# Optimization experiments

Measured on AMD Instinct MI355X. Metric: run time of the kernel, lower is better.

## Reference

```python
import jax, jax.numpy as jnp
import numpy as np

T, E, K, H, I = 1024, 8, 2, 1024, 2048  # tokens, experts, top_k, hidden, intermediate


def setup_inputs() -> dict:
    key = jax.random.key(0)
    k1, k2, k3, k4, k5 = jax.random.split(key, 5)
    x = jax.random.normal(k1, (T, H), dtype=jnp.float32)
    router_logits = jax.random.normal(k2, (T, E), dtype=jnp.float32)
    # expert weights: w1/w3 = gate/up proj (E,H,I); w2 = down proj (E,I,H)
    w1 = jax.random.normal(k3, (E, H, I), dtype=jnp.float32) / np.float32(np.sqrt(H))
    w3 = jax.random.normal(k4, (E, H, I), dtype=jnp.float32) / np.float32(np.sqrt(H))
    w2 = jax.random.normal(k5, (E, I, H), dtype=jnp.float32) / np.float32(np.sqrt(I))
    return {"x": x, "router_logits": router_logits, "w1": w1, "w3": w3, "w2": w2}


def reference(x, router_logits, w1, w3, w2):
    # --- fused top-k router (renormalize_topk_logits=False) ---
    probs = jax.nn.softmax(router_logits, axis=-1)          # [T, E]
    top_vals, top_ids = jax.lax.top_k(probs, K)             # [T, K]
    t_idx = jnp.arange(probs.shape[0])[:, None]
    # sparse combine weights scattered back to dense [T, E] (per-row ids are unique)
    gate = jnp.zeros_like(probs).at[t_idx, top_ids].add(top_vals)
    # --- expert FFN: silu(x@w1) * (x@w3) @ w2, masked by gate ---
    h = jnp.einsum('th,ehi->tei', x, w1)                    # [T, E, I]
    u = jnp.einsum('th,ehi->tei', x, w3)                    # [T, E, I]
    a = jax.nn.silu(h) * u                                  # [T, E, I]
    y = jnp.einsum('tei,eio->teo', a, w2)                   # [T, E, H]
    out = jnp.einsum('te,teo->to', gate, y)                 # [T, H]
    return out
```

## Files before the change

### kernel.cpp

```cpp
#include <hip/hip_runtime.h>

#define T_TOK 1024
#define NEXP 8
#define HID 1024
#define INTER 2048
#define SLOT_CAP 2176
#define NSLOT 2048
#define MAXTILES 24

#define BK 32
#define SPLITK 2
#define KCHUNK (INTER / SPLITK)

typedef __bf16 bf16x8 __attribute__((ext_vector_type(8)));
typedef float f32x4 __attribute__((ext_vector_type(4)));

typedef const __attribute__((address_space(1))) void gv_t;
typedef __attribute__((address_space(3))) void lv_t;
static __device__ __forceinline__ void dma16(const void* g, void* l) {
  __builtin_amdgcn_global_load_lds((gv_t*)g, (lv_t*)l, 16, 0, 0);
}
#define VMW(N) asm volatile("s_waitcnt vmcnt(" #N ")" ::: "memory")
#define LKW() asm volatile("s_waitcnt lgkmcnt(0)" ::: "memory")

#define WS_COUNTS 0
#define WS_OFFSETS 64
#define WS_TEXPERT 128
#define WS_TGATE (WS_TEXPERT + T_TOK * 2 * 4)
#define WS_TRANK (WS_TGATE + T_TOK * 2 * 4)
#define WS_TOKEN_OF (WS_TRANK + T_TOK * 2 * 4)
#define WS_GATE_OF (WS_TOKEN_OF + SLOT_CAP * 4)
#define WS_SLOT_OF (WS_GATE_OF + SLOT_CAP * 4)
#define WS_TILE_E (WS_SLOT_OF + T_TOK * 2 * 4)
#define WS_TILE_R (WS_TILE_E + 256)
#define WS_NTILES (WS_TILE_R + 256)
#define WS_ABUF 65536
#define WS_YS (WS_ABUF + SLOT_CAP * INTER * 2)

__global__ void moe_router(const float* __restrict__ logits, int* __restrict__ counts,
                           int* __restrict__ t_expert, float* __restrict__ t_gate,
                           int* __restrict__ t_rank) {
  int t = blockIdx.x * blockDim.x + threadIdx.x;
  if (t >= T_TOK) return;
  float l[NEXP];
  float mx = -1e30f;
#pragma unroll
  for (int e = 0; e < NEXP; ++e) {
    l[e] = logits[t * NEXP + e];
    mx = fmaxf(mx, l[e]);
  }
  float s = 0.f;
#pragma unroll
  for (int e = 0; e < NEXP; ++e) {
    l[e] = __expf(l[e] - mx);
    s += l[e];
  }
  float inv = 1.f / s;
  int i0 = 0;
#pragma unroll
  for (int e = 1; e < NEXP; ++e)
    if (l[e] > l[i0]) i0 = e;
  int i1 = (i0 == 0) ? 1 : 0;
#pragma unroll
  for (int e = 0; e < NEXP; ++e)
    if (e != i0 && e != i1 && l[e] > l[i1]) i1 = e;
  int es[2] = {i0, i1};
#pragma unroll
  for (int k = 0; k < 2; ++k) {
    int e = es[k];
    int r = atomicAdd(&counts[e], 1);
    int p = t * 2 + k;
    t_expert[p] = e;
    t_gate[p] = l[e] * inv;
    t_rank[p] = r;
  }
}

__global__ void moe_assign(const int* __restrict__ counts, int* __restrict__ offsets,
                           const int* __restrict__ t_expert, const float* __restrict__ t_gate,
                           const int* __restrict__ t_rank, int* __restrict__ token_of,
                           float* __restrict__ gate_of, int* __restrict__ slot_of,
                           int* __restrict__ tile_e, int* __restrict__ tile_r,
                           int* __restrict__ n_tiles) {
  __shared__ int off_s[NEXP];
  if (threadIdx.x == 0) {
    int s = 0, nt = 0;
    for (int e = 0; e < NEXP; ++e) {
      off_s[e] = s;
      offsets[e] = s;
      int ntile = (counts[e] + 127) >> 7;
      for (int r = 0; r < ntile; ++r) {
        tile_e[nt] = e;
        tile_r[nt] = r;
        ++nt;
      }
      s += counts[e];
    }
    *n_tiles = nt;
  }
  __syncthreads();
  for (int p = threadIdx.x; p < T_TOK * 2; p += blockDim.x) {
    int e = t_expert[p];
    int slot = off_s[e] + t_rank[p];
    token_of[slot] = p >> 1;
    gate_of[slot] = t_gate[p];
    slot_of[p] = slot;
  }
}

__global__ void moe_xgather(const float* __restrict__ x, const int* __restrict__ token_of,
                            __bf16* __restrict__ xg) {
  int idx = blockIdx.x * blockDim.x + threadIdx.x;
  int slot = idx >> 7;
  int c = (idx & 127) * 8;
  const float* src = x + (size_t)token_of[slot] * HID + c;
  float4 v0 = *(const float4*)src;
  float4 v1 = *(const float4*)(src + 4);
  bf16x8 o = {(__bf16)v0.x, (__bf16)v0.y, (__bf16)v0.z, (__bf16)v0.w,
              (__bf16)v1.x, (__bf16)v1.y, (__bf16)v1.z, (__bf16)v1.w};
  *(bf16x8*)&xg[(size_t)slot * HID + c] = o;
}

__global__ __launch_bounds__(256, 3) void moe_gemm1(
    const __bf16* __restrict__ xg, const float* __restrict__ w1, const float* __restrict__ w3,
    const int* __restrict__ offsets, const int* __restrict__ counts,
    const int* __restrict__ tile_e, const int* __restrict__ tile_r,
    const int* __restrict__ n_tiles, __bf16* __restrict__ abuf) {
  if ((int)blockIdx.y >= *n_tiles) return;
  const int e = tile_e[blockIdx.y];
  const int rt = tile_r[blockIdx.y];
  const int n_e = counts[e];
  const int off_e = offsets[e];
  const int col0 = blockIdx.x * 64;
  const int tid = threadIdx.x;
  const int lane = tid & 63;
  const int w = tid >> 6;
  const int wr = (w >> 1) * 64;
  const int wc = (w & 1) * 32;
  const int lr = lane & 15, lg = lane >> 4;

  __shared__ __align__(16) unsigned char sm[2 * 24576];

  f32x4 acc_h[4][2], acc_u[4][2];
#pragma unroll
  for (int m = 0; m < 4; ++m)
#pragma unroll
    for (int n = 0; n < 2; ++n) {
      acc_h[m][n] = (f32x4){0.f, 0.f, 0.f, 0.f};
      acc_u[m][n] = (f32x4){0.f, 0.f, 0.f, 0.f};
    }

  const int c0 = w * 2;
  const __bf16* aSrc[2];
#pragma unroll
  for (int j = 0; j < 2; ++j) {
    int row = (c0 + j) * 16 + (lane >> 2);
    int r_loc = rt * 128 + row;
    int slot = off_e + (r_loc < n_e ? r_loc : n_e - 1);
    aSrc[j] = xg + (size_t)slot * HID + (lane & 3) * 8;
  }
  const float* b1Src[2];
  const float* b3Src[2];
#pragma unroll
  for (int j = 0; j < 2; ++j) {
    int kr = (c0 + j) * 4 + (lane >> 4);
    int gsrc = (lane & 15) ^ ((kr >> 3) & 3);
    size_t rowoff = (size_t)kr * INTER + col0 + gsrc * 4;
    b1Src[j] = w1 + (size_t)e * HID * INTER + rowoff;
    b3Src[j] = w3 + (size_t)e * HID * INTER + rowoff;
  }

#define G1_ISSUE(S, K0)                                                        \
  {                                                                            \
    unsigned char* base = sm + (S)*24576;                                      \
    dma16(aSrc[0] + (K0), base + (c0 + 0) * 1024);                             \
    dma16(aSrc[1] + (K0), base + (c0 + 1) * 1024);                             \
    dma16(b1Src[0] + (size_t)(K0)*INTER, base + 8192 + (c0 + 0) * 1024);       \
    dma16(b1Src[1] + (size_t)(K0)*INTER, base + 8192 + (c0 + 1) * 1024);       \
    dma16(b3Src[0] + (size_t)(K0)*INTER, base + 16384 + (c0 + 0) * 1024);      \
    dma16(b3Src[1] + (size_t)(K0)*INTER, base + 16384 + (c0 + 1) * 1024);      \
  }

#define G1_BFRAG(dstf, matoff, N)                                              \
  bf16x8 dstf;                                                                 \
  {                                                                            \
    int col = wc + (N)*16 + lr;                                                \
    int boff = lg * 2048 + (((col >> 2) ^ lg) << 4) + ((col & 3) << 2);        \
    const unsigned char* bb = base + (matoff) + boff;                          \
    float v0 = *(const float*)(bb + 0 * 256), v1 = *(const float*)(bb + 1 * 256); \
    float v2 = *(const float*)(bb + 2 * 256), v3 = *(const float*)(bb + 3 * 256); \
    float v4 = *(const float*)(bb + 4 * 256), v5 = *(const float*)(bb + 5 * 256); \
    float v6 = *(const float*)(bb + 6 * 256), v7 = *(const float*)(bb + 7 * 256); \
    dstf = (bf16x8){(__bf16)v0, (__bf16)v1, (__bf16)v2, (__bf16)v3,            \
                    (__bf16)v4, (__bf16)v5, (__bf16)v6, (__bf16)v7};           \
  }

  const int NT = HID / BK;
  G1_ISSUE(0, 0);
  G1_ISSUE(1, BK);
  VMW(6);
  __builtin_amdgcn_s_barrier();

#pragma unroll 1
  for (int t = 0; t < NT; ++t) {
    const int s = t & 1;
    const unsigned char* base = sm + s * 24576;
    bf16x8 af[4];
#pragma unroll
    for (int m = 0; m < 4; ++m)
      af[m] = *(const bf16x8*)(base + (wr + m * 16 + lr) * 64 + lg * 16);
    G1_BFRAG(bf1a, 8192, 0);
    G1_BFRAG(bf1b, 8192, 1);
    G1_BFRAG(bf3a, 16384, 0);
    G1_BFRAG(bf3b, 16384, 1);
#pragma unroll
    for (int m = 0; m < 4; ++m) {
      acc_h[m][0] = __builtin_amdgcn_mfma_f32_16x16x32_bf16(af[m], bf1a, acc_h[m][0], 0, 0, 0);
      acc_h[m][1] = __builtin_amdgcn_mfma_f32_16x16x32_bf16(af[m], bf1b, acc_h[m][1], 0, 0, 0);
      acc_u[m][0] = __builtin_amdgcn_mfma_f32_16x16x32_bf16(af[m], bf3a, acc_u[m][0], 0, 0, 0);
      acc_u[m][1] = __builtin_amdgcn_mfma_f32_16x16x32_bf16(af[m], bf3b, acc_u[m][1], 0, 0, 0);
    }
    LKW();
    __builtin_amdgcn_s_barrier();
    if (t + 2 < NT) {
      G1_ISSUE(s, (t + 2) * BK);
      VMW(6);
    } else {
      VMW(0);
    }
    __builtin_amdgcn_s_barrier();
  }
#undef G1_ISSUE
#undef G1_BFRAG

#pragma unroll
  for (int m = 0; m < 4; ++m)
#pragma unroll
    for (int n = 0; n < 2; ++n) {
      int col = col0 + wc + n * 16 + lr;
#pragma unroll
      for (int r = 0; r < 4; ++r) {
        int row_loc = rt * 128 + wr + m * 16 + lg * 4 + r;
        if (row_loc < n_e) {
          float h = acc_h[m][n][r];
          float u = acc_u[m][n][r];
          float a = h / (1.f + __expf(-h)) * u;
          abuf[(size_t)(off_e + row_loc) * INTER + col] = (__bf16)a;
        }
      }
    }
}

__global__ __launch_bounds__(256, 4) void moe_gemm2(
    const __bf16* __restrict__ abuf, const float* __restrict__ w2,
    const int* __restrict__ offsets, const int* __restrict__ counts,
    const float* __restrict__ gate_of, const int* __restrict__ tile_e,
    const int* __restrict__ tile_r, const int* __restrict__ n_tiles,
    float* __restrict__ yslot) {
  if ((int)blockIdx.y >= *n_tiles) return;
  const int e = tile_e[blockIdx.y];
  const int rt = tile_r[blockIdx.y];
  const int sk = blockIdx.z;
  const int n_e = counts[e];
  const int off_e = offsets[e];
  const int col0 = blockIdx.x * 64;
  const int kbase = sk * KCHUNK;
  const int tid = threadIdx.x;
  const int lane = tid & 63;
  const int w = tid >> 6;
  const int wr = (w >> 1) * 64;
  const int wc = (w & 1) * 32;
  const int lr = lane & 15, lg = lane >> 4;

  __shared__ __align__(16) unsigned char sm[2 * 16384];

  f32x4 acc[4][2];
#pragma unroll
  for (int m = 0; m < 4; ++m)
#pragma unroll
    for (int n = 0; n < 2; ++n) acc[m][n] = (f32x4){0.f, 0.f, 0.f, 0.f};

  const int c0 = w * 2;
  const __bf16* aSrc[2];
#pragma unroll
  for (int j = 0; j < 2; ++j) {
    int row = (c0 + j) * 16 + (lane >> 2);
    int r_loc = rt * 128 + row;
    int slot = off_e + (r_loc < n_e ? r_loc : n_e - 1);
    aSrc[j] = abuf + (size_t)slot * INTER + kbase + (lane & 3) * 8;
  }
  const float* bSrc[2];
#pragma unroll
  for (int j = 0; j < 2; ++j) {
    int kr = (c0 + j) * 4 + (lane >> 4);
    int gsrc = (lane & 15) ^ ((kr >> 3) & 3);
    bSrc[j] = w2 + (size_t)e * INTER * HID + (size_t)(kbase + kr) * HID + col0 + gsrc * 4;
  }

#define G2_ISSUE(S, K0)                                                        \
  {                                                                            \
    unsigned char* base = sm + (S)*16384;                                      \
    dma16(aSrc[0] + (K0), base + (c0 + 0) * 1024);                             \
    dma16(aSrc[1] + (K0), base + (c0 + 1) * 1024);                             \
    dma16(bSrc[0] + (size_t)(K0)*HID, base + 8192 + (c0 + 0) * 1024);          \
    dma16(bSrc[1] + (size_t)(K0)*HID, base + 8192 + (c0 + 1) * 1024);          \
  }
#define G2_BFRAG(dstf, N)                                                      \
  bf16x8 dstf;                                                                 \
  {                                                                            \
    int col = wc + (N)*16 + lr;                                                \
    int boff = lg * 2048 + (((col >> 2) ^ lg) << 4) + ((col & 3) << 2);        \
    const unsigned char* bb = base + 8192 + boff;                              \
    float v0 = *(const float*)(bb + 0 * 256), v1 = *(const float*)(bb + 1 * 256); \
    float v2 = *(const float*)(bb + 2 * 256), v3 = *(const float*)(bb + 3 * 256); \
    float v4 = *(const float*)(bb + 4 * 256), v5 = *(const float*)(bb + 5 * 256); \
    float v6 = *(const float*)(bb + 6 * 256), v7 = *(const float*)(bb + 7 * 256); \
    dstf = (bf16x8){(__bf16)v0, (__bf16)v1, (__bf16)v2, (__bf16)v3,            \
                    (__bf16)v4, (__bf16)v5, (__bf16)v6, (__bf16)v7};           \
  }

  const int NT = KCHUNK / BK;
  G2_ISSUE(0, 0);
  G2_ISSUE(1, BK);
  VMW(4);
  __builtin_amdgcn_s_barrier();

#pragma unroll 1
  for (int t = 0; t < NT; ++t) {
    const int s = t & 1;
    const unsigned char* base = sm + s * 16384;
    bf16x8 af[4];
#pragma unroll
    for (int m = 0; m < 4; ++m)
      af[m] = *(const bf16x8*)(base + (wr + m * 16 + lr) * 64 + lg * 16);
    G2_BFRAG(bfa, 0);
    G2_BFRAG(bfb, 1);
#pragma unroll
    for (int m = 0; m < 4; ++m) {
      acc[m][0] = __builtin_amdgcn_mfma_f32_16x16x32_bf16(af[m], bfa, acc[m][0], 0, 0, 0);
      acc[m][1] = __builtin_amdgcn_mfma_f32_16x16x32_bf16(af[m], bfb, acc[m][1], 0, 0, 0);
    }
    LKW();
    __builtin_amdgcn_s_barrier();
    if (t + 2 < NT) {
      G2_ISSUE(s, (t + 2) * BK);
      VMW(4);
    } else {
      VMW(0);
    }
    __builtin_amdgcn_s_barrier();
  }
#undef G2_ISSUE
#undef G2_BFRAG

  float* ysk = yslot + (size_t)sk * NSLOT * HID;
#pragma unroll
  for (int m = 0; m < 4; ++m)
#pragma unroll
    for (int n = 0; n < 2; ++n) {
      int col = col0 + wc + n * 16 + lr;
#pragma unroll
      for (int r = 0; r < 4; ++r) {
        int row_loc = rt * 128 + wr + m * 16 + lg * 4 + r;
        if (row_loc < n_e) {
          int slot = off_e + row_loc;
          ysk[(size_t)slot * HID + col] = gate_of[slot] * acc[m][n][r];
        }
      }
    }
}

__global__ void moe_combine(const float* __restrict__ yslot, const int* __restrict__ slot_of,
                            float* __restrict__ out) {
  int i = blockIdx.x * blockDim.x + threadIdx.x;
  const int N4 = T_TOK * HID / 4;
  if (i >= N4) return;
  int t = i >> 8;
  int c4 = i & 255;
  int sA = slot_of[2 * t];
  int sB = slot_of[2 * t + 1];
  const float4* ys0 = (const float4*)yslot;
  const float4* ys1 = (const float4*)(yslot + (size_t)NSLOT * HID);
  float4 a = ys0[(size_t)sA * 256 + c4];
  float4 b = ys0[(size_t)sB * 256 + c4];
  float4 c = ys1[(size_t)sA * 256 + c4];
  float4 d = ys1[(size_t)sB * 256 + c4];
  float4 s;
  s.x = ((a.x + b.x) + c.x) + d.x;
  s.y = ((a.y + b.y) + c.y) + d.y;
  s.z = ((a.z + b.z) + c.z) + d.z;
  s.w = ((a.w + b.w) + c.w) + d.w;
  ((float4*)out)[i] = s;
}

extern "C" void kernel_launch(void* const* d_in, const int* in_sizes, int n_in,
                              void* d_out, int out_size, void* d_ws, size_t ws_size,
                              hipStream_t stream) {
  const float* x = (const float*)d_in[0];
  const float* logits = (const float*)d_in[1];
  const float* w1 = (const float*)d_in[2];
  const float* w3 = (const float*)d_in[3];
  const float* w2 = (const float*)d_in[4];
  float* out = (float*)d_out;
  char* ws = (char*)d_ws;

  int* counts = (int*)(ws + WS_COUNTS);
  int* offsets = (int*)(ws + WS_OFFSETS);
  int* t_expert = (int*)(ws + WS_TEXPERT);
  float* t_gate = (float*)(ws + WS_TGATE);
  int* t_rank = (int*)(ws + WS_TRANK);
  int* token_of = (int*)(ws + WS_TOKEN_OF);
  float* gate_of = (float*)(ws + WS_GATE_OF);
  int* slot_of = (int*)(ws + WS_SLOT_OF);
  int* tile_e = (int*)(ws + WS_TILE_E);
  int* tile_r = (int*)(ws + WS_TILE_R);
  int* n_tiles = (int*)(ws + WS_NTILES);
  __bf16* abuf = (__bf16*)(ws + WS_ABUF);
  float* yslot = (float*)(ws + WS_YS);
  __bf16* xg = (__bf16*)(ws + WS_YS);

  hipMemsetAsync(counts, 0, 64, stream);
  moe_router<<<dim3(4), dim3(256), 0, stream>>>(logits, counts, t_expert, t_gate, t_rank);
  moe_assign<<<dim3(1), dim3(256), 0, stream>>>(counts, offsets, t_expert, t_gate, t_rank,
                                                token_of, gate_of, slot_of, tile_e, tile_r,
                                                n_tiles);
  moe_xgather<<<dim3(NSLOT * (HID / 8) / 256), dim3(256), 0, stream>>>(x, token_of, xg);
  moe_gemm1<<<dim3(INTER / 64, MAXTILES), dim3(256), 0, stream>>>(
      xg, w1, w3, offsets, counts, tile_e, tile_r, n_tiles, abuf);
  moe_gemm2<<<dim3(HID / 64, MAXTILES, SPLITK), dim3(256), 0, stream>>>(
      abuf, w2, offsets, counts, gate_of, tile_e, tile_r, n_tiles, yslot);
  moe_combine<<<dim3((T_TOK * HID / 4 + 255) / 256), dim3(256), 0, stream>>>(yslot, slot_of,
                                                                             out);
}
```

Measured before the change: 111.2 us.

## Widen MoE GEMM tiles to 128 columns with 512-thread blocks and new B layout

```diff
diff --git a/kernel.cpp b/kernel.cpp
--- a/kernel.cpp
+++ b/kernel.cpp
@@ -121,7 +121,7 @@
   *(bf16x8*)&xg[(size_t)slot * HID + c] = o;
 }
 
-__global__ __launch_bounds__(256, 3) void moe_gemm1(
+__global__ __launch_bounds__(512, 4) void moe_gemm1(
     const __bf16* __restrict__ xg, const float* __restrict__ w1, const float* __restrict__ w3,
     const int* __restrict__ offsets, const int* __restrict__ counts,
     const int* __restrict__ tile_e, const int* __restrict__ tile_r,
@@ -131,15 +131,15 @@
   const int rt = tile_r[blockIdx.y];
   const int n_e = counts[e];
   const int off_e = offsets[e];
-  const int col0 = blockIdx.x * 64;
+  const int col0 = blockIdx.x * 128;
   const int tid = threadIdx.x;
   const int lane = tid & 63;
   const int w = tid >> 6;
-  const int wr = (w >> 1) * 64;
-  const int wc = (w & 1) * 32;
+  const int wr = (w >> 2) * 64;
+  const int wc = (w & 3) * 32;
   const int lr = lane & 15, lg = lane >> 4;
 
-  __shared__ __align__(16) unsigned char sm[2 * 24576];
+  __shared__ __align__(16) unsigned char sm[2 * 40960];
 
   f32x4 acc_h[4][2], acc_u[4][2];
 #pragma unroll
@@ -150,47 +150,45 @@
       acc_u[m][n] = (f32x4){0.f, 0.f, 0.f, 0.f};
     }
 
-  const int c0 = w * 2;
-  const __bf16* aSrc[2];
-#pragma unroll
-  for (int j = 0; j < 2; ++j) {
-    int row = (c0 + j) * 16 + (lane >> 2);
+  const __bf16* aSrc;
+  {
+    int row = w * 16 + (lane >> 2);
     int r_loc = rt * 128 + row;
     int slot = off_e + (r_loc < n_e ? r_loc : n_e - 1);
-    aSrc[j] = xg + (size_t)slot * HID + (lane & 3) * 8;
+    aSrc = xg + (size_t)slot * HID + (lane & 3) * 8;
   }
   const float* b1Src[2];
   const float* b3Src[2];
 #pragma unroll
-  for (int j = 0; j < 2; ++j) {
-    int kr = (c0 + j) * 4 + (lane >> 4);
-    int gsrc = (lane & 15) ^ ((kr >> 3) & 3);
-    size_t rowoff = (size_t)kr * INTER + col0 + gsrc * 4;
-    b1Src[j] = w1 + (size_t)e * HID * INTER + rowoff;
-    b3Src[j] = w3 + (size_t)e * HID * INTER + rowoff;
+  for (int j2 = 0; j2 < 2; ++j2) {
+    int c = w * 2 + j2;
+    int kr = (lane & 3) * 8 + (c >> 1);
+    int cg = (c & 1) * 16 + (lane >> 2);
+    size_t rowoff = (size_t)kr * INTER + col0 + cg * 4;
+    b1Src[j2] = w1 + (size_t)e * HID * INTER + rowoff;
+    b3Src[j2] = w3 + (size_t)e * HID * INTER + rowoff;
   }
 
 #define G1_ISSUE(S, K0)                                                        \
   {                                                                            \
-    unsigned char* base = sm + (S)*24576;                                      \
-    dma16(aSrc[0] + (K0), base + (c0 + 0) * 1024);                             \
-    dma16(aSrc[1] + (K0), base + (c0 + 1) * 1024);                             \
-    dma16(b1Src[0] + (size_t)(K0)*INTER, base + 8192 + (c0 + 0) * 1024);       \
-    dma16(b1Src[1] + (size_t)(K0)*INTER, base + 8192 + (c0 + 1) * 1024);       \
-    dma16(b3Src[0] + (size_t)(K0)*INTER, base + 16384 + (c0 + 0) * 1024);      \
-    dma16(b3Src[1] + (size_t)(K0)*INTER, base + 16384 + (c0 + 1) * 1024);      \
+    unsigned char* base = sm + (S)*40960;                                      \
+    dma16(aSrc + (K0), base + w * 1024);                                       \
+    dma16(b1Src[0] + (size_t)(K0)*INTER, base + 8192 + (w * 2 + 0) * 1024);    \
+    dma16(b1Src[1] + (size_t)(K0)*INTER, base + 8192 + (w * 2 + 1) * 1024);    \
+    dma16(b3Src[0] + (size_t)(K0)*INTER, base + 24576 + (w * 2 + 0) * 1024);   \
+    dma16(b3Src[1] + (size_t)(K0)*INTER, base + 24576 + (w * 2 + 1) * 1024);   \
   }
 
 #define G1_BFRAG(dstf, matoff, N)                                              \
   bf16x8 dstf;                                                                 \
   {                                                                            \
     int col = wc + (N)*16 + lr;                                                \
-    int boff = lg * 2048 + (((col >> 2) ^ lg) << 4) + ((col & 3) << 2);        \
-    const unsigned char* bb = base + (matoff) + boff;                          \
-    float v0 = *(const float*)(bb + 0 * 256), v1 = *(const float*)(bb + 1 * 256); \
-    float v2 = *(const float*)(bb + 2 * 256), v3 = *(const float*)(bb + 3 * 256); \
-    float v4 = *(const float*)(bb + 4 * 256), v5 = *(const float*)(bb + 5 * 256); \
-    float v6 = *(const float*)(bb + 6 * 256), v7 = *(const float*)(bb + 7 * 256); \
+    const unsigned char* bb =                                                  \
+        base + (matoff) + (col >> 2) * 64 + lg * 16 + (col & 3) * 4;           \
+    float v0 = *(const float*)(bb + 0 * 2048), v1 = *(const float*)(bb + 1 * 2048); \
+    float v2 = *(const float*)(bb + 2 * 2048), v3 = *(const float*)(bb + 3 * 2048); \
+    float v4 = *(const float*)(bb + 4 * 2048), v5 = *(const float*)(bb + 5 * 2048); \
+    float v6 = *(const float*)(bb + 6 * 2048), v7 = *(const float*)(bb + 7 * 2048); \
     dstf = (bf16x8){(__bf16)v0, (__bf16)v1, (__bf16)v2, (__bf16)v3,            \
                     (__bf16)v4, (__bf16)v5, (__bf16)v6, (__bf16)v7};           \
   }
@@ -198,21 +196,21 @@
   const int NT = HID / BK;
   G1_ISSUE(0, 0);
   G1_ISSUE(1, BK);
-  VMW(6);
+  VMW(5);
   __builtin_amdgcn_s_barrier();
 
 #pragma unroll 1
   for (int t = 0; t < NT; ++t) {
     const int s = t & 1;
-    const unsigned char* base = sm + s * 24576;
+    const unsigned char* base = sm + s * 40960;
     bf16x8 af[4];
 #pragma unroll
     for (int m = 0; m < 4; ++m)
       af[m] = *(const bf16x8*)(base + (wr + m * 16 + lr) * 64 + lg * 16);
     G1_BFRAG(bf1a, 8192, 0);
     G1_BFRAG(bf1b, 8192, 1);
-    G1_BFRAG(bf3a, 16384, 0);
-    G1_BFRAG(bf3b, 16384, 1);
+    G1_BFRAG(bf3a, 24576, 0);
+    G1_BFRAG(bf3b, 24576, 1);
 #pragma unroll
     for (int m = 0; m < 4; ++m) {
       acc_h[m][0] = __builtin_amdgcn_mfma_f32_16x16x32_bf16(af[m], bf1a, acc_h[m][0], 0, 0, 0);
@@ -224,7 +222,7 @@
     __builtin_amdgcn_s_barrier();
     if (t + 2 < NT) {
       G1_ISSUE(s, (t + 2) * BK);
-      VMW(6);
+      VMW(5);
     } else {
       VMW(0);
     }
@@ -251,7 +249,7 @@
     }
 }
 
-__global__ __launch_bounds__(256, 4) void moe_gemm2(
+__global__ __launch_bounds__(512, 4) void moe_gemm2(
     const __bf16* __restrict__ abuf, const float* __restrict__ w2,
     const int* __restrict__ offsets, const int* __restrict__ counts,
     const float* __restrict__ gate_of, const int* __restrict__ tile_e,
@@ -263,16 +261,16 @@
   const int sk = blockIdx.z;
   const int n_e = counts[e];
   const int off_e = offsets[e];
-  const int col0 = blockIdx.x * 64;
+  const int col0 = blockIdx.x * 128;
   const int kbase = sk * KCHUNK;
   const int tid = threadIdx.x;
   const int lane = tid & 63;
   const int w = tid >> 6;
-  const int wr = (w >> 1) * 64;
-  const int wc = (w & 1) * 32;
+  const int wr = (w >> 2) * 64;
+  const int wc = (w & 3) * 32;
   const int lr = lane & 15, lg = lane >> 4;
 
-  __shared__ __align__(16) unsigned char sm[2 * 16384];
+  __shared__ __align__(16) unsigned char sm[2 * 24576];
 
   f32x4 acc[4][2];
 #pragma unroll
@@ -280,41 +278,39 @@
 #pragma unroll
     for (int n = 0; n < 2; ++n) acc[m][n] = (f32x4){0.f, 0.f, 0.f, 0.f};
 
-  const int c0 = w * 2;
-  const __bf16* aSrc[2];
-#pragma unroll
-  for (int j = 0; j < 2; ++j) {
-    int row = (c0 + j) * 16 + (lane >> 2);
+  const __bf16* aSrc;
+  {
+    int row = w * 16 + (lane >> 2);
     int r_loc = rt * 128 + row;
     int slot = off_e + (r_loc < n_e ? r_loc : n_e - 1);
-    aSrc[j] = abuf + (size_t)slot * INTER + kbase + (lane & 3) * 8;
+    aSrc = abuf + (size_t)slot * INTER + kbase + (lane & 3) * 8;
   }
   const float* bSrc[2];
 #pragma unroll
-  for (int j = 0; j < 2; ++j) {
-    int kr = (c0 + j) * 4 + (lane >> 4);
-    int gsrc = (lane & 15) ^ ((kr >> 3) & 3);
-    bSrc[j] = w2 + (size_t)e * INTER * HID + (size_t)(kbase + kr) * HID + col0 + gsrc * 4;
+  for (int j2 = 0; j2 < 2; ++j2) {
+    int c = w * 2 + j2;
+    int kr = (lane & 3) * 8 + (c >> 1);
+    int cg = (c & 1) * 16 + (lane >> 2);
+    bSrc[j2] = w2 + (size_t)e * INTER * HID + (size_t)(kbase + kr) * HID + col0 + cg * 4;
   }
 
 #define G2_ISSUE(S, K0)                                                        \
   {                                                                            \
-    unsigned char* base = sm + (S)*16384;                                      \
-    dma16(aSrc[0] + (K0), base + (c0 + 0) * 1024);                             \
-    dma16(aSrc[1] + (K0), base + (c0 + 1) * 1024);                             \
-    dma16(bSrc[0] + (size_t)(K0)*HID, base + 8192 + (c0 + 0) * 1024);          \
-    dma16(bSrc[1] + (size_t)(K0)*HID, base + 8192 + (c0 + 1) * 1024);          \
+    unsigned char* base = sm + (S)*24576;                                      \
+    dma16(aSrc + (K0), base + w * 1024);                                       \
+    dma16(bSrc[0] + (size_t)(K0)*HID, base + 8192 + (w * 2 + 0) * 1024);       \
+    dma16(bSrc[1] + (size_t)(K0)*HID, base + 8192 + (w * 2 + 1) * 1024);       \
   }
 #define G2_BFRAG(dstf, N)                                                      \
   bf16x8 dstf;                                                                 \
   {                                                                            \
     int col = wc + (N)*16 + lr;                                                \
-    int boff = lg * 2048 + (((col >> 2) ^ lg) << 4) + ((col & 3) << 2);        \
-    const unsigned char* bb = base + 8192 + boff;                              \
-    float v0 = *(const float*)(bb + 0 * 256), v1 = *(const float*)(bb + 1 * 256); \
-    float v2 = *(const float*)(bb + 2 * 256), v3 = *(const float*)(bb + 3 * 256); \
-    float v4 = *(const float*)(bb + 4 * 256), v5 = *(const float*)(bb + 5 * 256); \
-    float v6 = *(const float*)(bb + 6 * 256), v7 = *(const float*)(bb + 7 * 256); \
+    const unsigned char* bb =                                                  \
+        base + 8192 + (col >> 2) * 64 + lg * 16 + (col & 3) * 4;               \
+    float v0 = *(const float*)(bb + 0 * 2048), v1 = *(const float*)(bb + 1 * 2048); \
+    float v2 = *(const float*)(bb + 2 * 2048), v3 = *(const float*)(bb + 3 * 2048); \
+    float v4 = *(const float*)(bb + 4 * 2048), v5 = *(const float*)(bb + 5 * 2048); \
+    float v6 = *(const float*)(bb + 6 * 2048), v7 = *(const float*)(bb + 7 * 2048); \
     dstf = (bf16x8){(__bf16)v0, (__bf16)v1, (__bf16)v2, (__bf16)v3,            \
                     (__bf16)v4, (__bf16)v5, (__bf16)v6, (__bf16)v7};           \
   }
@@ -322,13 +318,13 @@
   const int NT = KCHUNK / BK;
   G2_ISSUE(0, 0);
   G2_ISSUE(1, BK);
-  VMW(4);
+  VMW(3);
   __builtin_amdgcn_s_barrier();
 
 #pragma unroll 1
   for (int t = 0; t < NT; ++t) {
     const int s = t & 1;
-    const unsigned char* base = sm + s * 16384;
+    const unsigned char* base = sm + s * 24576;
     bf16x8 af[4];
 #pragma unroll
     for (int m = 0; m < 4; ++m)
@@ -344,7 +340,7 @@
     __builtin_amdgcn_s_barrier();
     if (t + 2 < NT) {
       G2_ISSUE(s, (t + 2) * BK);
-      VMW(4);
+      VMW(3);
     } else {
       VMW(0);
     }
@@ -425,9 +421,9 @@
                                                 token_of, gate_of, slot_of, tile_e, tile_r,
                                                 n_tiles);
   moe_xgather<<<dim3(NSLOT * (HID / 8) / 256), dim3(256), 0, stream>>>(x, token_of, xg);
-  moe_gemm1<<<dim3(INTER / 64, MAXTILES), dim3(256), 0, stream>>>(
+  moe_gemm1<<<dim3(INTER / 128, MAXTILES), dim3(512), 0, stream>>>(
       xg, w1, w3, offsets, counts, tile_e, tile_r, n_tiles, abuf);
-  moe_gemm2<<<dim3(HID / 64, MAXTILES, SPLITK), dim3(256), 0, stream>>>(
+  moe_gemm2<<<dim3(HID / 128, MAXTILES, SPLITK), dim3(512), 0, stream>>>(
       abuf, w2, offsets, counts, gate_of, tile_e, tile_r, n_tiles, yslot);
   moe_combine<<<dim3((T_TOK * HID / 4 + 255) / 256), dim3(256), 0, stream>>>(yslot, slot_of,
                                                                              out);
```

Result: slower. 151.0 us (+35.7%).
